# Performance work log

Hardware: AMD Instinct MI355X
Metric: run time of the kernel (lower is better)

## Reference

```python
import jax, jax.numpy as jnp
import numpy as np


def setup_inputs() -> dict:
    key = jax.random.key(0)
    k1, k2, k3 = jax.random.split(key, 3)
    N1, N2, P, D = 4, 8, 1024, 128  # P = PH*PW = 32*32 (512px / 16 patch)
    feats = jax.random.normal(k1, (N1, P, D), dtype=jnp.float32)
    nfeats = jax.random.normal(k2, (N2, P, D), dtype=jnp.float32)
    background_masks = jax.random.uniform(k3, (N1, P), dtype=jnp.float32)
    return {"feats": feats, "nfeats": nfeats, "background_masks": background_masks,
            "PH": 32, "PW": 32, "H": 512, "W": 512}


def reference(feats, nfeats, background_masks, PH, PW, H, W):
    # L2-normalize patch embeddings (as in `f / f.norm(dim=-1, keepdim=True)`)
    f = feats / jnp.linalg.norm(feats, axis=-1, keepdims=True)    # [N1,P,D]
    g = nfeats / jnp.linalg.norm(nfeats, axis=-1, keepdims=True)  # [N2,Q,D]
    # Euclidean cdist of unit vectors: d^2 = 2 - 2*dot (clamped at 0)
    dot = jnp.einsum('npd,mqd->nmpq', f, g)                        # [N1,N2,P,Q]
    dist = jnp.sqrt(jnp.maximum(2.0 - 2.0 * dot, 0.0)) / 2.0      # cdist/2, permuted
    # min over normal patches Q -> per-query-patch nearest-neighbor distance
    scores_patch = dist.min(axis=-1)                               # [N1,N2,P]
    scores_patch = scores_patch * background_masks[:, None, :]
    # image score: max over query patches, mean over normal images
    scores = scores_patch.max(axis=-1).mean(axis=-1)               # [N1]
    # pixel map: mean over normal images, reshape to patch grid, bilinear upsample
    sp = scores_patch.mean(axis=1).reshape(-1, PH, PW)             # [N1,PH,PW]
    scores_pixel = jax.image.resize(sp, (sp.shape[0], H, W), method='bilinear')
    return scores, scores_pixel
```

## Files before the change

### kernel.cpp

```cpp
#include <hip/hip_runtime.h>

typedef __attribute__((ext_vector_type(8))) short short8;
typedef __attribute__((ext_vector_type(4))) float f32x4;
typedef __attribute__((ext_vector_type(4))) unsigned int u32x4;

static __device__ inline unsigned short f2bf(float x) {
    unsigned int u = __float_as_uint(x);
    u = (u + 0x7FFFu + ((u >> 16) & 1u)) >> 16;
    return (unsigned short)u;
}

static __device__ inline unsigned int pk(float a, float b, float inv) {
    return (unsigned int)f2bf(a * inv) | ((unsigned int)f2bf(b * inv) << 16);
}

__global__ __launch_bounds__(256, 2) void kscore(const float* __restrict__ feats,
                                                 const float* __restrict__ nfeats,
                                                 float* __restrict__ sp_part) {
    __shared__ char gtile[2][8192];
    const int tid = threadIdx.x;
    const int lane = tid & 63;
    const int wave = tid >> 6;
    const int l15 = lane & 15, lhi = lane >> 4;
    const int m = blockIdx.x;
    const int ptile = blockIdx.y >> 2, qq = blockIdx.y & 3;
    const int rowbase = ptile * 256 + wave * 64;

    const float* gBase = nfeats + ((size_t)m * 1024 + qq * 256) * 128;

    const int r0 = tid >> 4, s0 = tid & 15;
    const int r1 = r0 + 16;
    const float* gsrc0 = gBase + (size_t)r0 * 128 + s0 * 8;
    const float* gsrc1 = gBase + (size_t)r1 * 128 + s0 * 8;
    const int wofs0 = (r0 * 256 + s0 * 16) ^ ((r0 & 7) << 4);
    const int wofs1 = (r1 * 256 + s0 * 16) ^ ((r1 & 7) << 4);

    auto ldrow = [](const float* p, f32x4& x, f32x4& y) {
        x = *(const f32x4*)(p);
        y = *(const f32x4*)(p + 4);
    };
    auto rownorm = [&](const f32x4& x, const f32x4& y) {
        float ss = x[0]*x[0] + x[1]*x[1] + x[2]*x[2] + x[3]*x[3]
                 + y[0]*y[0] + y[1]*y[1] + y[2]*y[2] + y[3]*y[3];
        ss += __shfl_xor(ss, 1);
        ss += __shfl_xor(ss, 2);
        ss += __shfl_xor(ss, 4);
        ss += __shfl_xor(ss, 8);
        return 1.0f / sqrtf(ss);
    };
    auto packrow = [&](const f32x4& x, const f32x4& y, float inv) {
        u32x4 o;
        o.x = pk(x[0], x[1], inv);
        o.y = pk(x[2], x[3], inv);
        o.z = pk(y[0], y[1], inv);
        o.w = pk(y[2], y[3], inv);
        return o;
    };

    f32x4 t0xa, t0ya, t0xb, t0yb, t1xa, t1ya, t1xb, t1yb;
    ldrow(gsrc0, t0xa, t0ya); ldrow(gsrc1, t0xb, t0yb);
    ldrow(gsrc0 + 32 * 128, t1xa, t1ya); ldrow(gsrc1 + 32 * 128, t1xb, t1yb);

    short8 a[4][4];
    #pragma unroll
    for (int pg = 0; pg < 4; pg++) {
        const float* arow = feats + (size_t)(rowbase + pg * 16 + l15) * 128 + lhi * 8;
        f32x4 vx[4], vy[4];
        float ss = 0.f;
        #pragma unroll
        for (int kk = 0; kk < 4; kk++) {
            vx[kk] = *(const f32x4*)(arow + kk * 32);
            vy[kk] = *(const f32x4*)(arow + kk * 32 + 4);
            #pragma unroll
            for (int j = 0; j < 4; j++) ss += vx[kk][j]*vx[kk][j] + vy[kk][j]*vy[kk][j];
        }
        ss += __shfl_xor(ss, 16);
        ss += __shfl_xor(ss, 32);
        float inv = 1.0f / sqrtf(ss);
        #pragma unroll
        for (int kk = 0; kk < 4; kk++) {
            u32x4 o = packrow(vx[kk], vy[kk], inv);
            a[pg][kk] = *(short8*)&o;
        }
    }

    {
        float i0 = rownorm(t0xa, t0ya);
        *(u32x4*)(gtile[0] + wofs0) = packrow(t0xa, t0ya, i0);
        float i1 = rownorm(t0xb, t0yb);
        *(u32x4*)(gtile[0] + wofs1) = packrow(t0xb, t0yb, i1);
    }

    f32x4 mx[4];
    #pragma unroll
    for (int pg = 0; pg < 4; pg++)
        #pragma unroll
        for (int i = 0; i < 4; i++) mx[pg][i] = -1e30f;

    asm volatile("s_waitcnt lgkmcnt(0)" ::: "memory");
    __builtin_amdgcn_s_barrier();

    #pragma unroll
    for (int t = 0; t < 8; t++) {
        __builtin_amdgcn_sched_barrier(0);
        f32x4 n2xa, n2ya, n2xb, n2yb;
        if (t < 6) {
            ldrow(gsrc0 + (size_t)(t + 2) * 32 * 128, n2xa, n2ya);
            ldrow(gsrc1 + (size_t)(t + 2) * 32 * 128, n2xb, n2yb);
        }
        if (t < 7) {
            float i0 = rownorm(t1xa, t1ya);
            *(u32x4*)(gtile[(t + 1) & 1] + wofs0) = packrow(t1xa, t1ya, i0);
            float i1 = rownorm(t1xb, t1yb);
            *(u32x4*)(gtile[(t + 1) & 1] + wofs1) = packrow(t1xb, t1yb, i1);
        }
        const char* tp = gtile[t & 1];
        #pragma unroll
        for (int qt = 0; qt < 2; qt++) {
            const int r = qt * 16 + l15;
            const int rowoff = r * 256;
            const int swz = (r & 7) << 4;
            f32x4 acc[4];
            #pragma unroll
            for (int pg = 0; pg < 4; pg++)
                #pragma unroll
                for (int i = 0; i < 4; i++) acc[pg][i] = 0.f;
            #pragma unroll
            for (int kk = 0; kk < 4; kk++) {
                short8 b = *(const short8*)(tp + ((rowoff + kk * 64 + lhi * 16) ^ swz));
                #pragma unroll
                for (int pg = 0; pg < 4; pg++)
                    acc[pg] = __builtin_amdgcn_mfma_f32_16x16x32_bf16(a[pg][kk], b, acc[pg], 0, 0, 0);
            }
            #pragma unroll
            for (int pg = 0; pg < 4; pg++)
                #pragma unroll
                for (int i = 0; i < 4; i++) mx[pg][i] = fmaxf(mx[pg][i], acc[pg][i]);
        }
        if (t < 6) { t1xa = n2xa; t1ya = n2ya; t1xb = n2xb; t1yb = n2yb; }
        asm volatile("s_waitcnt lgkmcnt(0)" ::: "memory");
        __builtin_amdgcn_s_barrier();
    }

    #pragma unroll
    for (int pg = 0; pg < 4; pg++)
        #pragma unroll
        for (int i = 0; i < 4; i++) {
            float v = mx[pg][i];
            v = fmaxf(v, __shfl_xor(v, 1));
            v = fmaxf(v, __shfl_xor(v, 2));
            v = fmaxf(v, __shfl_xor(v, 4));
            v = fmaxf(v, __shfl_xor(v, 8));
            mx[pg][i] = v;
        }
    if (l15 == 0) {
        #pragma unroll
        for (int pg = 0; pg < 4; pg++)
            #pragma unroll
            for (int i = 0; i < 4; i++) {
                int row = rowbase + pg * 16 + lhi * 4 + i;
                int n = row >> 10, p = row & 1023;
                sp_part[((size_t)(n * 8 + m) * 4 + qq) * 1024 + p] = mx[pg][i];
            }
    }
}

__global__ __launch_bounds__(256) void kfinal(const float* __restrict__ sp_part,
                                              const float* __restrict__ mask,
                                              float* __restrict__ out) {
    const int n = blockIdx.y;
    const int bx = blockIdx.x;
    const int t = threadIdx.x;
    float* pix = out + 4;

    if (bx == 64) {
        __shared__ float smax[4];
        float acc = 0.f;
        for (int m = 0; m < 8; m++) {
            const float* base = sp_part + (size_t)(n * 8 + m) * 4 * 1024;
            float lm = -1e30f;
            #pragma unroll
            for (int i = 0; i < 4; i++) {
                int p = i * 256 + t;
                float dot = fmaxf(fmaxf(base[p], base[1024 + p]),
                                  fmaxf(base[2048 + p], base[3072 + p]));
                float d = sqrtf(fmaxf(2.0f - 2.0f * dot, 0.0f)) * 0.5f * mask[n * 1024 + p];
                lm = fmaxf(lm, d);
            }
            #pragma unroll
            for (int d = 32; d; d >>= 1) lm = fmaxf(lm, __shfl_xor(lm, d));
            if ((t & 63) == 0) smax[t >> 6] = lm;
            __syncthreads();
            if (t == 0) acc += fmaxf(fmaxf(smax[0], smax[1]), fmaxf(smax[2], smax[3]));
            __syncthreads();
        }
        if (t == 0) out[n] = acc * 0.125f;
        return;
    }

    __shared__ float sp_row[2][32];
    const int band = bx * 8;
    const int pr_lo = (int)floorf((band + 0.5f) * 0.0625f - 0.5f);
    const int row0 = min(max(pr_lo, 0), 31);
    const int row1 = min(max(pr_lo + 1, 0), 31);
    {
        int v = t >> 2, sub = t & 3;
        int vr = v >> 5, vc = v & 31;
        int p = (vr ? row1 : row0) * 32 + vc;
        float sum = 0.f;
        #pragma unroll
        for (int mi = 0; mi < 2; mi++) {
            int m = sub * 2 + mi;
            const float* base = sp_part + (size_t)(n * 8 + m) * 4 * 1024 + p;
            float dot = fmaxf(fmaxf(base[0], base[1024]),
                              fmaxf(base[2048], base[3072]));
            sum += sqrtf(fmaxf(2.0f - 2.0f * dot, 0.0f)) * 0.5f;
        }
        sum *= mask[n * 1024 + p];
        sum += __shfl_xor(sum, 1);
        sum += __shfl_xor(sum, 2);
        if (sub == 0) sp_row[vr][vc] = sum * 0.125f;
    }
    __syncthreads();
    #pragma unroll
    for (int i = 0; i < 16; i++) {
        int idx = i * 256 + t;
        int yl = idx >> 9, x = idx & 511;
        int y = band + yl;
        float fy = (y + 0.5f) * 0.0625f - 0.5f;
        float ty = fy - (float)pr_lo;
        float fx = (x + 0.5f) * 0.0625f - 0.5f;
        float xf = floorf(fx);
        float tx = fx - xf;
        int x0 = (int)xf;
        int x0c = min(max(x0, 0), 31), x1c = min(max(x0 + 1, 0), 31);
        float v00 = sp_row[0][x0c], v01 = sp_row[0][x1c];
        float v10 = sp_row[1][x0c], v11 = sp_row[1][x1c];
        float v0 = v00 + tx * (v01 - v00);
        float v1 = v10 + tx * (v11 - v10);
        pix[(size_t)n * 262144 + (size_t)y * 512 + x] = v0 + ty * (v1 - v0);
    }
}

extern "C" void kernel_launch(void* const* d_in, const int* in_sizes, int n_in,
                              void* d_out, int out_size, void* d_ws, size_t ws_size,
                              hipStream_t stream) {
    const float* feats = (const float*)d_in[0];
    const float* nfeats = (const float*)d_in[1];
    const float* mask = (const float*)d_in[2];
    float* out = (float*)d_out;

    float* sp_part = (float*)d_ws;

    kscore<<<dim3(8, 64), 256, 0, stream>>>(feats, nfeats, sp_part);
    kfinal<<<dim3(65, 4), 256, 0, stream>>>(sp_part, mask, out);
}
```

Before: 33.91 us.

## Stage whole 256-row normal tile in LDS once instead of double-buffered pipeline

Replaces the 8-step double-buffered LDS pipeline (32 rows per step with a barrier each step) with a single phase that loads, normalizes and packs all 256 normal rows into a 64 KB LDS tile, followed by one barrier and a 16-iteration MFMA loop. This removes the per-step barriers and the software-pipelining bookkeeping. In exchange it gives up overlap between global loads and MFMA work. The larger LDS footprint may also limit how many blocks fit per CU, even though launch bounds still request 2.

```diff
diff --git a/kernel.cpp b/kernel.cpp
--- a/kernel.cpp
+++ b/kernel.cpp
@@ -17,7 +17,7 @@
 __global__ __launch_bounds__(256, 2) void kscore(const float* __restrict__ feats,
                                                  const float* __restrict__ nfeats,
                                                  float* __restrict__ sp_part) {
-    __shared__ char gtile[2][8192];
+    __shared__ char gtile[256 * 256];
     const int tid = threadIdx.x;
     const int lane = tid & 63;
     const int wave = tid >> 6;
@@ -28,39 +28,6 @@
 
     const float* gBase = nfeats + ((size_t)m * 1024 + qq * 256) * 128;
 
-    const int r0 = tid >> 4, s0 = tid & 15;
-    const int r1 = r0 + 16;
-    const float* gsrc0 = gBase + (size_t)r0 * 128 + s0 * 8;
-    const float* gsrc1 = gBase + (size_t)r1 * 128 + s0 * 8;
-    const int wofs0 = (r0 * 256 + s0 * 16) ^ ((r0 & 7) << 4);
-    const int wofs1 = (r1 * 256 + s0 * 16) ^ ((r1 & 7) << 4);
-
-    auto ldrow = [](const float* p, f32x4& x, f32x4& y) {
-        x = *(const f32x4*)(p);
-        y = *(const f32x4*)(p + 4);
-    };
-    auto rownorm = [&](const f32x4& x, const f32x4& y) {
-        float ss = x[0]*x[0] + x[1]*x[1] + x[2]*x[2] + x[3]*x[3]
-                 + y[0]*y[0] + y[1]*y[1] + y[2]*y[2] + y[3]*y[3];
-        ss += __shfl_xor(ss, 1);
-        ss += __shfl_xor(ss, 2);
-        ss += __shfl_xor(ss, 4);
-        ss += __shfl_xor(ss, 8);
-        return 1.0f / sqrtf(ss);
-    };
-    auto packrow = [&](const f32x4& x, const f32x4& y, float inv) {
-        u32x4 o;
-        o.x = pk(x[0], x[1], inv);
-        o.y = pk(x[2], x[3], inv);
-        o.z = pk(y[0], y[1], inv);
-        o.w = pk(y[2], y[3], inv);
-        return o;
-    };
-
-    f32x4 t0xa, t0ya, t0xb, t0yb, t1xa, t1ya, t1xb, t1yb;
-    ldrow(gsrc0, t0xa, t0ya); ldrow(gsrc1, t0xb, t0yb);
-    ldrow(gsrc0 + 32 * 128, t1xa, t1ya); ldrow(gsrc1 + 32 * 128, t1xb, t1yb);
-
     short8 a[4][4];
     #pragma unroll
     for (int pg = 0; pg < 4; pg++) {
@@ -79,17 +46,41 @@
         float inv = 1.0f / sqrtf(ss);
         #pragma unroll
         for (int kk = 0; kk < 4; kk++) {
-            u32x4 o = packrow(vx[kk], vy[kk], inv);
+            u32x4 o;
+            o.x = pk(vx[kk][0], vx[kk][1], inv);
+            o.y = pk(vx[kk][2], vx[kk][3], inv);
+            o.z = pk(vy[kk][0], vy[kk][1], inv);
+            o.w = pk(vy[kk][2], vy[kk][3], inv);
             a[pg][kk] = *(short8*)&o;
         }
     }
 
     {
-        float i0 = rownorm(t0xa, t0ya);
-        *(u32x4*)(gtile[0] + wofs0) = packrow(t0xa, t0ya, i0);
-        float i1 = rownorm(t0xb, t0yb);
-        *(u32x4*)(gtile[0] + wofs1) = packrow(t0xb, t0yb, i1);
-    }
+        const int s0 = tid & 15;
+        const int rb = tid >> 4;
+        #pragma unroll
+        for (int b = 0; b < 16; b++) {
+            const int r = rb + b * 16;
+            const float* src = gBase + (size_t)r * 128 + s0 * 8;
+            f32x4 x = *(const f32x4*)(src);
+            f32x4 y = *(const f32x4*)(src + 4);
+            float ss = x[0]*x[0] + x[1]*x[1] + x[2]*x[2] + x[3]*x[3]
+                     + y[0]*y[0] + y[1]*y[1] + y[2]*y[2] + y[3]*y[3];
+            ss += __shfl_xor(ss, 1);
+            ss += __shfl_xor(ss, 2);
+            ss += __shfl_xor(ss, 4);
+            ss += __shfl_xor(ss, 8);
+            float inv = 1.0f / sqrtf(ss);
+            u32x4 o;
+            o.x = pk(x[0], x[1], inv);
+            o.y = pk(x[2], x[3], inv);
+            o.z = pk(y[0], y[1], inv);
+            o.w = pk(y[2], y[3], inv);
+            *(u32x4*)(gtile + ((r * 256 + s0 * 16) ^ ((r & 7) << 4))) = o;
+        }
+    }
+
+    __syncthreads();
 
     f32x4 mx[4];
     #pragma unroll
@@ -97,49 +88,29 @@
         #pragma unroll
         for (int i = 0; i < 4; i++) mx[pg][i] = -1e30f;
 
-    asm volatile("s_waitcnt lgkmcnt(0)" ::: "memory");
-    __builtin_amdgcn_s_barrier();
-
-    #pragma unroll
-    for (int t = 0; t < 8; t++) {
-        __builtin_amdgcn_sched_barrier(0);
-        f32x4 n2xa, n2ya, n2xb, n2yb;
-        if (t < 6) {
-            ldrow(gsrc0 + (size_t)(t + 2) * 32 * 128, n2xa, n2ya);
-            ldrow(gsrc1 + (size_t)(t + 2) * 32 * 128, n2xb, n2yb);
-        }
-        if (t < 7) {
-            float i0 = rownorm(t1xa, t1ya);
-            *(u32x4*)(gtile[(t + 1) & 1] + wofs0) = packrow(t1xa, t1ya, i0);
-            float i1 = rownorm(t1xb, t1yb);
-            *(u32x4*)(gtile[(t + 1) & 1] + wofs1) = packrow(t1xb, t1yb, i1);
-        }
-        const char* tp = gtile[t & 1];
-        #pragma unroll
-        for (int qt = 0; qt < 2; qt++) {
-            const int r = qt * 16 + l15;
-            const int rowoff = r * 256;
-            const int swz = (r & 7) << 4;
-            f32x4 acc[4];
-            #pragma unroll
-            for (int pg = 0; pg < 4; pg++)
-                #pragma unroll
-                for (int i = 0; i < 4; i++) acc[pg][i] = 0.f;
-            #pragma unroll
-            for (int kk = 0; kk < 4; kk++) {
-                short8 b = *(const short8*)(tp + ((rowoff + kk * 64 + lhi * 16) ^ swz));
-                #pragma unroll
-                for (int pg = 0; pg < 4; pg++)
-                    acc[pg] = __builtin_amdgcn_mfma_f32_16x16x32_bf16(a[pg][kk], b, acc[pg], 0, 0, 0);
-            }
-            #pragma unroll
-            for (int pg = 0; pg < 4; pg++)
-                #pragma unroll
-                for (int i = 0; i < 4; i++) mx[pg][i] = fmaxf(mx[pg][i], acc[pg][i]);
-        }
-        if (t < 6) { t1xa = n2xa; t1ya = n2ya; t1xb = n2xb; t1yb = n2yb; }
-        asm volatile("s_waitcnt lgkmcnt(0)" ::: "memory");
-        __builtin_amdgcn_s_barrier();
+    #pragma unroll
+    for (int qt = 0; qt < 16; qt++) {
+        const int r = qt * 16 + l15;
+        const int rowoff = r * 256;
+        const int swz = (r & 7) << 4;
+        short8 b0 = *(const short8*)(gtile + ((rowoff +   0 + lhi * 16) ^ swz));
+        short8 b1 = *(const short8*)(gtile + ((rowoff +  64 + lhi * 16) ^ swz));
+        short8 b2 = *(const short8*)(gtile + ((rowoff + 128 + lhi * 16) ^ swz));
+        short8 b3 = *(const short8*)(gtile + ((rowoff + 192 + lhi * 16) ^ swz));
+        f32x4 acc[4];
+        #pragma unroll
+        for (int pg = 0; pg < 4; pg++) {
+            #pragma unroll
+            for (int i = 0; i < 4; i++) acc[pg][i] = 0.f;
+            acc[pg] = __builtin_amdgcn_mfma_f32_16x16x32_bf16(a[pg][0], b0, acc[pg], 0, 0, 0);
+            acc[pg] = __builtin_amdgcn_mfma_f32_16x16x32_bf16(a[pg][1], b1, acc[pg], 0, 0, 0);
+            acc[pg] = __builtin_amdgcn_mfma_f32_16x16x32_bf16(a[pg][2], b2, acc[pg], 0, 0, 0);
+            acc[pg] = __builtin_amdgcn_mfma_f32_16x16x32_bf16(a[pg][3], b3, acc[pg], 0, 0, 0);
+        }
+        #pragma unroll
+        for (int pg = 0; pg < 4; pg++)
+            #pragma unroll
+            for (int i = 0; i < 4; i++) mx[pg][i] = fmaxf(mx[pg][i], acc[pg][i]);
     }
 
     #pragma unroll
```

New measurement: 34.87 us. +2.8%, slower.
